# Performance work log

Measured on AMD Instinct MI355X. Metric: run time of the kernel, lower is better.

Reference implementation:

```python
import jax, jax.numpy as jnp
import numpy as np

N_NODES = 100000
IN_FEATURES = 5000
OUT_FEATURES = 64
NNZ = 4000000


def setup_inputs() -> dict:
    key = jax.random.key(0)
    k_row, k_col, k_val, k_w, k_b = jax.random.split(key, 5)
    rows = jax.random.randint(k_row, (NNZ,), 0, N_NODES, dtype=jnp.int64 if jax.config.jax_enable_x64 else jnp.int32)
    cols = jax.random.randint(k_col, (NNZ,), 0, IN_FEATURES, dtype=rows.dtype)
    index = jnp.stack([rows, cols], axis=0)  # [2, nnz] COO
    value = jax.random.uniform(k_val, (NNZ,), dtype=jnp.float32)
    # kaiming_uniform_(mode='fan_out', a=sqrt(5)) on [in, out]: fan_out = out_features
    gain = np.sqrt(2.0 / (1.0 + 5.0))
    bound_w = gain * np.sqrt(3.0 / OUT_FEATURES)
    weight = jax.random.uniform(k_w, (IN_FEATURES, OUT_FEATURES), jnp.float32, -bound_w, bound_w)
    bound_b = 1.0 / np.sqrt(OUT_FEATURES)
    bias = jax.random.uniform(k_b, (OUT_FEATURES,), jnp.float32, -bound_b, bound_b)
    return {"index": index, "value": value, "n": N_NODES, "weight": weight, "bias": bias}


def reference(index, value, n, weight, bias):
    # spmm: out[r, :] = sum over nnz with row==r of value * weight[col, :]
    rows, cols = index[0], index[1]
    contrib = value[:, None] * weight[cols]            # [nnz, out] gather + scale
    res = jax.ops.segment_sum(contrib, rows, num_segments=n)  # [n, out] scatter-add
    return res + bias[None, :]
```

## Files before the change

### kernel.cpp

```cpp
#include <hip/hip_runtime.h>


#define NBF 1024
#define DMAX 128
#define CH 8192
#define CC 1536
#define SP_T 512

__device__ __forceinline__ void ds_fadd(float* p, float v) {
    unsigned a = (unsigned)(unsigned long long)p;
    asm volatile("ds_add_f32 %0, %1" :: "v"(a), "v"(v) : "memory");
}

__global__ __launch_bounds__(1024) void k_bin_fixed(const int* __restrict__ rows,
        const int* __restrict__ cols, const float* __restrict__ vals, int nnz,
        unsigned M, int S, int d, int slots, int* __restrict__ cntF,
        unsigned long long* __restrict__ pairs1, int* __restrict__ ovfCnt,
        unsigned long long* __restrict__ ovf) {
    __shared__ unsigned long long stage[CH];
    __shared__ int histF[NBF], scF[NBF], adjF[NBF];
    __shared__ int wsum[16];
    int t = threadIdx.x, lane = t & 63, wv = t >> 6;
    long long base = (long long)blockIdx.x * CH;
    int count = (int)min((long long)CH, (long long)nnz - base);
    histF[t] = 0;
    __syncthreads();
    int f8[8], rk8[8];
    unsigned long long pk8[8];
    if (count == CH) {
        const int4*   r4 = (const int4*)(rows + base);
        const int4*   c4 = (const int4*)(cols + base);
        const float4* v4 = (const float4*)(vals + base);
        int4 ra = r4[t * 2], rb = r4[t * 2 + 1];
        int4 ca = c4[t * 2], cb = c4[t * 2 + 1];
        float4 va = v4[t * 2], vb = v4[t * 2 + 1];
        int   rr[8] = {ra.x, ra.y, ra.z, ra.w, rb.x, rb.y, rb.z, rb.w};
        int   cc[8] = {ca.x, ca.y, ca.z, ca.w, cb.x, cb.y, cb.z, cb.w};
        float vv[8] = {va.x, va.y, va.z, va.w, vb.x, vb.y, vb.z, vb.w};
#pragma unroll
        for (int k = 0; k < 8; ++k) {
            unsigned r = (unsigned)rr[k];
            int f = (int)(((unsigned long long)r * M) >> S);
            int lr = (int)r - f * d;
            f8[k] = f;
            rk8[k] = atomicAdd(&histF[f], 1);
            pk8[k] = ((unsigned long long)__float_as_uint(vv[k]) << 32) |
                     ((unsigned)f << 20) | ((unsigned)lr << 13) | (unsigned)cc[k];
        }
    } else {
#pragma unroll
        for (int k = 0; k < 8; ++k) {
            int i = t + (k << 10);
            f8[k] = -1;
            if (i < count) {
                unsigned r = (unsigned)rows[base + i];
                int c = cols[base + i];
                float vv = vals[base + i];
                int f = (int)(((unsigned long long)r * M) >> S);
                int lr = (int)r - f * d;
                f8[k] = f;
                rk8[k] = atomicAdd(&histF[f], 1);
                pk8[k] = ((unsigned long long)__float_as_uint(vv) << 32) |
                         ((unsigned)f << 20) | ((unsigned)lr << 13) | (unsigned)c;
            }
        }
    }
    __syncthreads();
    int v = histF[t], x = v;
#pragma unroll
    for (int off = 1; off < 64; off <<= 1) {
        int y = __shfl_up(x, off, 64);
        if (lane >= off) x += y;
    }
    if (lane == 63) wsum[wv] = x;
    __syncthreads();
    if (t < 16) {
        int s = wsum[t], xs = s;
#pragma unroll
        for (int off = 1; off < 16; off <<= 1) {
            int y = __shfl_up(xs, off, 16);
            if (t >= off) xs += y;
        }
        wsum[t] = xs - s;
    }
    __syncthreads();
    int incl = x + wsum[wv];
    scF[t] = incl;
    if (v > 0) {
        int g = atomicAdd(&cntF[t], v);
        adjF[t] = t * slots + g - (incl - v);
    }
    __syncthreads();
#pragma unroll
    for (int k = 0; k < 8; ++k)
        if (f8[k] >= 0) stage[(scF[f8[k]] - histF[f8[k]]) + rk8[k]] = pk8[k];
    __syncthreads();
    for (int i = t; i < count; i += 1024) {
        unsigned long long p = stage[i];
        int f = (int)((p >> 20) & 1023);
        int dest = adjF[f] + i;
        if (dest < (f + 1) * slots) pairs1[dest] = p;
        else ovf[atomicAdd(ovfCnt, 1)] = p;
    }
}

__global__ __launch_bounds__(SP_T, 8) void k_spmm9(
        const unsigned long long* __restrict__ pairs, const int* __restrict__ cntF,
        const int* __restrict__ ovfCnt, const unsigned long long* __restrict__ ovf,
        const float* __restrict__ weight, const float* __restrict__ bias,
        float* __restrict__ out, int d, int n, int slots) {
    __shared__ unsigned long long stage[CC];
    __shared__ int histR[DMAX], scR[DMAX];
    extern __shared__ float acc[];
    int b = blockIdx.x, t = threadIdx.x;
    int row0 = b * d;
    if (row0 >= n) return;
    int nrows = min(d, n - row0);
    long long sbase = (long long)b * slots;
    int cnt = cntF[b];
    if (cnt > slots) cnt = slots;
    if (cnt < 0) cnt = 0;

    for (int i = t; i < (nrows << 6); i += SP_T) acc[i] = 0.0f;

    int g = t >> 4, fq = t & 15;
    for (int cb = 0; cb < cnt; cb += CC) {
        int ccnt = min(CC, cnt - cb);
        if (t < DMAX) histR[t] = 0;
        __syncthreads();
        int lr3[3], rk3[3];
        unsigned long long pk3[3];
#pragma unroll
        for (int k = 0; k < 3; ++k) {
            int i = t + (k << 9);
            lr3[k] = -1;
            if (i < ccnt) {
                unsigned long long p = pairs[sbase + cb + i];
                int lr = (int)((p >> 13) & 127);
                lr3[k] = lr;
                rk3[k] = atomicAdd(&histR[lr], 1);
                pk3[k] = p;
            }
        }
        __syncthreads();
        if (t < DMAX) {
            int v = histR[t], x = v;
            int lane = t & 63;
#pragma unroll
            for (int off = 1; off < 64; off <<= 1) {
                int y = __shfl_up(x, off, 64);
                if (lane >= off) x += y;
            }
            scR[t] = x;
        }
        __syncthreads();
        if (t >= 64 && t < DMAX) scR[t] += scR[63];
        __syncthreads();
#pragma unroll
        for (int k = 0; k < 3; ++k)
            if (lr3[k] >= 0) stage[(scR[lr3[k]] - histR[lr3[k]]) + rk3[k]] = pk3[k];
        __syncthreads();

        for (int r = g; r < nrows; r += 32) {
            int e = scR[r], s = e - histR[r];
            if (s >= e) continue;
            float4 a = {0.0f, 0.0f, 0.0f, 0.0f};
            int j = s;
            for (; j + 4 <= e; j += 4) {
                unsigned long long p0 = stage[j + 0];
                unsigned long long p1 = stage[j + 1];
                unsigned long long p2 = stage[j + 2];
                unsigned long long p3 = stage[j + 3];
                const float4 w0 = *(const float4*)(weight + (((int)(p0 & 8191)) << 6) + (fq << 2));
                const float4 w1 = *(const float4*)(weight + (((int)(p1 & 8191)) << 6) + (fq << 2));
                const float4 w2 = *(const float4*)(weight + (((int)(p2 & 8191)) << 6) + (fq << 2));
                const float4 w3 = *(const float4*)(weight + (((int)(p3 & 8191)) << 6) + (fq << 2));
                float v0 = __uint_as_float((unsigned)(p0 >> 32));
                float v1 = __uint_as_float((unsigned)(p1 >> 32));
                float v2 = __uint_as_float((unsigned)(p2 >> 32));
                float v3 = __uint_as_float((unsigned)(p3 >> 32));
                a.x = fmaf(v0, w0.x, a.x); a.y = fmaf(v0, w0.y, a.y);
                a.z = fmaf(v0, w0.z, a.z); a.w = fmaf(v0, w0.w, a.w);
                a.x = fmaf(v1, w1.x, a.x); a.y = fmaf(v1, w1.y, a.y);
                a.z = fmaf(v1, w1.z, a.z); a.w = fmaf(v1, w1.w, a.w);
                a.x = fmaf(v2, w2.x, a.x); a.y = fmaf(v2, w2.y, a.y);
                a.z = fmaf(v2, w2.z, a.z); a.w = fmaf(v2, w2.w, a.w);
                a.x = fmaf(v3, w3.x, a.x); a.y = fmaf(v3, w3.y, a.y);
                a.z = fmaf(v3, w3.z, a.z); a.w = fmaf(v3, w3.w, a.w);
            }
            for (; j < e; ++j) {
                unsigned long long p = stage[j];
                float vv = __uint_as_float((unsigned)(p >> 32));
                const float4 w = *(const float4*)(weight + (((int)(p & 8191)) << 6) + (fq << 2));
                a.x = fmaf(vv, w.x, a.x); a.y = fmaf(vv, w.y, a.y);
                a.z = fmaf(vv, w.z, a.z); a.w = fmaf(vv, w.w, a.w);
            }
            float4* ap = (float4*)&acc[(r << 6) + (fq << 2)];
            float4 o = *ap;
            o.x += a.x; o.y += a.y; o.z += a.z; o.w += a.w;
            *ap = o;
        }
        __syncthreads();
    }

    int oc = *ovfCnt;
    if (oc > 0) {
        __syncthreads();
        for (int i = g; i < oc; i += (SP_T >> 4)) {
            unsigned long long p = ovf[i];
            if ((int)((p >> 20) & 1023) == b) {
                int lr = (int)((p >> 13) & 127);
                int cc = (int)(p & 8191);
                float vv = __uint_as_float((unsigned)(p >> 32));
                const float4 w = *(const float4*)(weight + (cc << 6) + (fq << 2));
                float* ap = &acc[(lr << 6) + (fq << 2)];
                ds_fadd(ap + 0, vv * w.x); ds_fadd(ap + 1, vv * w.y);
                ds_fadd(ap + 2, vv * w.z); ds_fadd(ap + 3, vv * w.w);
            }
        }
        asm volatile("s_waitcnt lgkmcnt(0)" ::: "memory");
        __builtin_amdgcn_sched_barrier(0);
        __syncthreads();
    }

    for (int i = t; i < (nrows << 6); i += SP_T)
        out[((long long)row0 << 6) + i] = acc[i] + bias[i & 63];
}

extern "C" void kernel_launch(void* const* d_in, const int* in_sizes, int n_in,
                              void* d_out, int out_size, void* d_ws, size_t ws_size,
                              hipStream_t stream) {
    const int*   index  = (const int*)d_in[0];
    const float* value  = (const float*)d_in[1];
    const float* weight = (const float*)d_in[3];
    const float* bias   = (const float*)d_in[4];
    float*       out    = (float*)d_out;

    int nnz = in_sizes[0] / 2;
    int n   = out_size / 64;
    const int* rows = index;
    const int* cols = index + nnz;

    int d = (n + NBF - 1) / NBF;
    unsigned M = 0;
    int S = 0;
    for (S = 20; S <= 40; ++S) {
        unsigned long long m = ((1ull << S) + (unsigned)d - 1) / (unsigned)d;
        unsigned long long e = m * (unsigned long long)d - (1ull << S);
        if (m <= 0xffffffffull && e * (unsigned long long)(n > 0 ? n - 1 : 0) < (1ull << S)) {
            M = (unsigned)m;
            break;
        }
    }

    int nChunks = (nnz + CH - 1) / CH;
    char* ws = (char*)d_ws;
    int* cntF   = (int*)ws;
    int* ovfCnt = (int*)(ws + 4096);
    unsigned long long* pairsS = (unsigned long long*)(ws + (128 << 10));

    size_t szOvf = (((size_t)nnz * 8) + 255) & ~(size_t)255;
    size_t availS = (ws_size > (128 << 10) + szOvf) ? (ws_size - (128 << 10) - szOvf) : 0;
    long long slotsL = (long long)(availS / ((size_t)NBF * 8));
    int slots = (int)(slotsL > 6144 ? 6144 : slotsL);
    if (slots > 64) slots &= ~63;
    if (slots < 1) slots = 1;
    unsigned long long* ovf = (unsigned long long*)(ws + (128 << 10) + (size_t)slots * NBF * 8);

    hipMemsetAsync(ws, 0, 8192, stream);
    k_bin_fixed<<<nChunks, 1024, 0, stream>>>(rows, cols, value, nnz, M, S, d, slots,
                                              cntF, pairsS, ovfCnt, ovf);
    size_t smem = (size_t)d * 64 * sizeof(float);
    k_spmm9<<<NBF, SP_T, smem, stream>>>(pairsS, cntF, ovfCnt, ovf, weight, bias,
                                         out, d, n, slots);
}
```

Before: 160.6 us.

## Keep row accumulators in registers and enlarge SpMM staging chunk

Replaces the shared-memory per-row accumulator in the SpMM kernel with four float4 register accumulators per thread, each thread owning fixed rows (g + 32k), and writes output directly with bias. The staging chunk grows from 1536 to 4608 pairs. The first pass now keeps only the rank and local row in registers and re-reads the pair from global memory during the scatter. This removes LDS accumulator traffic and the dynamic shared allocation, and cuts the number of chunk iterations and barriers. In exchange it assumes at most 128 rows per block, adds a redundant global load per pair, and makes every thread scan the whole overflow list serially. The larger stage array (about 36KB) may also reduce occupancy.

Result: no change. 160.3 us (-0.2%).

```diff
diff --git a/kernel.cpp b/kernel.cpp
--- a/kernel.cpp
+++ b/kernel.cpp
@@ -4,13 +4,8 @@
 #define NBF 1024
 #define DMAX 128
 #define CH 8192
-#define CC 1536
+#define CC 4608
 #define SP_T 512
-
-__device__ __forceinline__ void ds_fadd(float* p, float v) {
-    unsigned a = (unsigned)(unsigned long long)p;
-    asm volatile("ds_add_f32 %0, %1" :: "v"(a), "v"(v) : "memory");
-}
 
 __global__ __launch_bounds__(1024) void k_bin_fixed(const int* __restrict__ rows,
         const int* __restrict__ cols, const float* __restrict__ vals, int nnz,
@@ -104,14 +99,13 @@
     }
 }
 
-__global__ __launch_bounds__(SP_T, 8) void k_spmm9(
+__global__ __launch_bounds__(SP_T, 8) void k_spmm12(
         const unsigned long long* __restrict__ pairs, const int* __restrict__ cntF,
         const int* __restrict__ ovfCnt, const unsigned long long* __restrict__ ovf,
         const float* __restrict__ weight, const float* __restrict__ bias,
         float* __restrict__ out, int d, int n, int slots) {
     __shared__ unsigned long long stage[CC];
     __shared__ int histR[DMAX], scR[DMAX];
-    extern __shared__ float acc[];
     int b = blockIdx.x, t = threadIdx.x;
     int row0 = b * d;
     if (row0 >= n) return;
@@ -121,25 +115,24 @@
     if (cnt > slots) cnt = slots;
     if (cnt < 0) cnt = 0;
 
-    for (int i = t; i < (nrows << 6); i += SP_T) acc[i] = 0.0f;
-
     int g = t >> 4, fq = t & 15;
+    const float* wbase = weight + (fq << 2);
+    float4 a0 = {0,0,0,0}, a1 = {0,0,0,0}, a2 = {0,0,0,0}, a3 = {0,0,0,0};
+
     for (int cb = 0; cb < cnt; cb += CC) {
         int ccnt = min(CC, cnt - cb);
         if (t < DMAX) histR[t] = 0;
         __syncthreads();
-        int lr3[3], rk3[3];
-        unsigned long long pk3[3];
-#pragma unroll
-        for (int k = 0; k < 3; ++k) {
+        int pr9[9];
+#pragma unroll
+        for (int k = 0; k < 9; ++k) {
             int i = t + (k << 9);
-            lr3[k] = -1;
+            pr9[k] = -1;
             if (i < ccnt) {
                 unsigned long long p = pairs[sbase + cb + i];
                 int lr = (int)((p >> 13) & 127);
-                lr3[k] = lr;
-                rk3[k] = atomicAdd(&histR[lr], 1);
-                pk3[k] = p;
+                int rk = atomicAdd(&histR[lr], 1);
+                pr9[k] = (rk << 7) | lr;
             }
         }
         __syncthreads();
@@ -157,74 +150,96 @@
         if (t >= 64 && t < DMAX) scR[t] += scR[63];
         __syncthreads();
 #pragma unroll
-        for (int k = 0; k < 3; ++k)
-            if (lr3[k] >= 0) stage[(scR[lr3[k]] - histR[lr3[k]]) + rk3[k]] = pk3[k];
-        __syncthreads();
-
-        for (int r = g; r < nrows; r += 32) {
-            int e = scR[r], s = e - histR[r];
-            if (s >= e) continue;
-            float4 a = {0.0f, 0.0f, 0.0f, 0.0f};
-            int j = s;
-            for (; j + 4 <= e; j += 4) {
-                unsigned long long p0 = stage[j + 0];
-                unsigned long long p1 = stage[j + 1];
-                unsigned long long p2 = stage[j + 2];
-                unsigned long long p3 = stage[j + 3];
-                const float4 w0 = *(const float4*)(weight + (((int)(p0 & 8191)) << 6) + (fq << 2));
-                const float4 w1 = *(const float4*)(weight + (((int)(p1 & 8191)) << 6) + (fq << 2));
-                const float4 w2 = *(const float4*)(weight + (((int)(p2 & 8191)) << 6) + (fq << 2));
-                const float4 w3 = *(const float4*)(weight + (((int)(p3 & 8191)) << 6) + (fq << 2));
-                float v0 = __uint_as_float((unsigned)(p0 >> 32));
-                float v1 = __uint_as_float((unsigned)(p1 >> 32));
-                float v2 = __uint_as_float((unsigned)(p2 >> 32));
-                float v3 = __uint_as_float((unsigned)(p3 >> 32));
-                a.x = fmaf(v0, w0.x, a.x); a.y = fmaf(v0, w0.y, a.y);
-                a.z = fmaf(v0, w0.z, a.z); a.w = fmaf(v0, w0.w, a.w);
-                a.x = fmaf(v1, w1.x, a.x); a.y = fmaf(v1, w1.y, a.y);
-                a.z = fmaf(v1, w1.z, a.z); a.w = fmaf(v1, w1.w, a.w);
-                a.x = fmaf(v2, w2.x, a.x); a.y = fmaf(v2, w2.y, a.y);
-                a.z = fmaf(v2, w2.z, a.z); a.w = fmaf(v2, w2.w, a.w);
-                a.x = fmaf(v3, w3.x, a.x); a.y = fmaf(v3, w3.y, a.y);
-                a.z = fmaf(v3, w3.z, a.z); a.w = fmaf(v3, w3.w, a.w);
-            }
-            for (; j < e; ++j) {
-                unsigned long long p = stage[j];
-                float vv = __uint_as_float((unsigned)(p >> 32));
-                const float4 w = *(const float4*)(weight + (((int)(p & 8191)) << 6) + (fq << 2));
-                a.x = fmaf(vv, w.x, a.x); a.y = fmaf(vv, w.y, a.y);
-                a.z = fmaf(vv, w.z, a.z); a.w = fmaf(vv, w.w, a.w);
-            }
-            float4* ap = (float4*)&acc[(r << 6) + (fq << 2)];
-            float4 o = *ap;
-            o.x += a.x; o.y += a.y; o.z += a.z; o.w += a.w;
-            *ap = o;
-        }
+        for (int k = 0; k < 9; ++k) {
+            if (pr9[k] >= 0) {
+                int i = t + (k << 9);
+                int lr = pr9[k] & 127, rk = pr9[k] >> 7;
+                stage[(scR[lr] - histR[lr]) + rk] = pairs[sbase + cb + i];
+            }
+        }
+        __syncthreads();
+
+#define CONSUME_ROW(K)                                                        \
+        {                                                                     \
+            int r = g + (K << 5);                                             \
+            if (r < nrows) {                                                  \
+                int e = scR[r], s = e - histR[r];                             \
+                float4 a = {0,0,0,0};                                         \
+                int j = s;                                                    \
+                for (; j + 4 <= e; j += 4) {                                  \
+                    unsigned long long p0 = stage[j + 0];                     \
+                    unsigned long long p1 = stage[j + 1];                     \
+                    unsigned long long p2 = stage[j + 2];                     \
+                    unsigned long long p3 = stage[j + 3];                     \
+                    const float4 w0 = *(const float4*)(wbase + ((int)(p0 & 8191) << 6)); \
+                    const float4 w1 = *(const float4*)(wbase + ((int)(p1 & 8191) << 6)); \
+                    const float4 w2 = *(const float4*)(wbase + ((int)(p2 & 8191) << 6)); \
+                    const float4 w3 = *(const float4*)(wbase + ((int)(p3 & 8191) << 6)); \
+                    float v0 = __uint_as_float((unsigned)(p0 >> 32));         \
+                    float v1 = __uint_as_float((unsigned)(p1 >> 32));         \
+                    float v2 = __uint_as_float((unsigned)(p2 >> 32));         \
+                    float v3 = __uint_as_float((unsigned)(p3 >> 32));         \
+                    a.x = fmaf(v0, w0.x, a.x); a.y = fmaf(v0, w0.y, a.y);     \
+                    a.z = fmaf(v0, w0.z, a.z); a.w = fmaf(v0, w0.w, a.w);     \
+                    a.x = fmaf(v1, w1.x, a.x); a.y = fmaf(v1, w1.y, a.y);     \
+                    a.z = fmaf(v1, w1.z, a.z); a.w = fmaf(v1, w1.w, a.w);     \
+                    a.x = fmaf(v2, w2.x, a.x); a.y = fmaf(v2, w2.y, a.y);     \
+                    a.z = fmaf(v2, w2.z, a.z); a.w = fmaf(v2, w2.w, a.w);     \
+                    a.x = fmaf(v3, w3.x, a.x); a.y = fmaf(v3, w3.y, a.y);     \
+                    a.z = fmaf(v3, w3.z, a.z); a.w = fmaf(v3, w3.w, a.w);     \
+                }                                                             \
+                for (; j < e; ++j) {                                          \
+                    unsigned long long p = stage[j];                          \
+                    float vv = __uint_as_float((unsigned)(p >> 32));          \
+                    const float4 w = *(const float4*)(wbase + ((int)(p & 8191) << 6)); \
+                    a.x = fmaf(vv, w.x, a.x); a.y = fmaf(vv, w.y, a.y);       \
+                    a.z = fmaf(vv, w.z, a.z); a.w = fmaf(vv, w.w, a.w);       \
+                }                                                             \
+                a##K.x += a.x; a##K.y += a.y; a##K.z += a.z; a##K.w += a.w;   \
+            }                                                                 \
+        }
+        CONSUME_ROW(0) CONSUME_ROW(1) CONSUME_ROW(2) CONSUME_ROW(3)
+#undef CONSUME_ROW
         __syncthreads();
     }
 
     int oc = *ovfCnt;
     if (oc > 0) {
-        __syncthreads();
-        for (int i = g; i < oc; i += (SP_T >> 4)) {
+        for (int i = 0; i < oc; ++i) {
             unsigned long long p = ovf[i];
             if ((int)((p >> 20) & 1023) == b) {
                 int lr = (int)((p >> 13) & 127);
-                int cc = (int)(p & 8191);
-                float vv = __uint_as_float((unsigned)(p >> 32));
-                const float4 w = *(const float4*)(weight + (cc << 6) + (fq << 2));
-                float* ap = &acc[(lr << 6) + (fq << 2)];
-                ds_fadd(ap + 0, vv * w.x); ds_fadd(ap + 1, vv * w.y);
-                ds_fadd(ap + 2, vv * w.z); ds_fadd(ap + 3, vv * w.w);
-            }
-        }
-        asm volatile("s_waitcnt lgkmcnt(0)" ::: "memory");
-        __builtin_amdgcn_sched_barrier(0);
-        __syncthreads();
-    }
-
-    for (int i = t; i < (nrows << 6); i += SP_T)
-        out[((long long)row0 << 6) + i] = acc[i] + bias[i & 63];
+                if ((lr & 31) == g) {
+                    int cc = (int)(p & 8191);
+                    float vv = __uint_as_float((unsigned)(p >> 32));
+                    const float4 w = *(const float4*)(wbase + (cc << 6));
+                    int k = lr >> 5;
+                    if (k == 0) { a0.x = fmaf(vv, w.x, a0.x); a0.y = fmaf(vv, w.y, a0.y);
+                                  a0.z = fmaf(vv, w.z, a0.z); a0.w = fmaf(vv, w.w, a0.w); }
+                    else if (k == 1) { a1.x = fmaf(vv, w.x, a1.x); a1.y = fmaf(vv, w.y, a1.y);
+                                  a1.z = fmaf(vv, w.z, a1.z); a1.w = fmaf(vv, w.w, a1.w); }
+                    else if (k == 2) { a2.x = fmaf(vv, w.x, a2.x); a2.y = fmaf(vv, w.y, a2.y);
+                                  a2.z = fmaf(vv, w.z, a2.z); a2.w = fmaf(vv, w.w, a2.w); }
+                    else { a3.x = fmaf(vv, w.x, a3.x); a3.y = fmaf(vv, w.y, a3.y);
+                                  a3.z = fmaf(vv, w.z, a3.z); a3.w = fmaf(vv, w.w, a3.w); }
+                }
+            }
+        }
+    }
+
+    float4 b4 = *(const float4*)(bias + (fq << 2));
+#define WRITE_ROW(K)                                                          \
+    {                                                                         \
+        int r = g + (K << 5);                                                 \
+        if (r < nrows) {                                                      \
+            float4 o;                                                         \
+            o.x = a##K.x + b4.x; o.y = a##K.y + b4.y;                         \
+            o.z = a##K.z + b4.z; o.w = a##K.w + b4.w;                         \
+            *(float4*)(out + (((long long)(row0 + r)) << 6) + (fq << 2)) = o; \
+        }                                                                     \
+    }
+    WRITE_ROW(0) WRITE_ROW(1) WRITE_ROW(2) WRITE_ROW(3)
+#undef WRITE_ROW
 }
 
 extern "C" void kernel_launch(void* const* d_in, const int* in_sizes, int n_in,
@@ -270,7 +285,6 @@
     hipMemsetAsync(ws, 0, 8192, stream);
     k_bin_fixed<<<nChunks, 1024, 0, stream>>>(rows, cols, value, nnz, M, S, d, slots,
                                               cntF, pairsS, ovfCnt, ovf);
-    size_t smem = (size_t)d * 64 * sizeof(float);
-    k_spmm9<<<NBF, SP_T, smem, stream>>>(pairsS, cntF, ovfCnt, ovf, weight, bias,
-                                         out, d, n, slots);
+    k_spmm12<<<NBF, SP_T, 0, stream>>>(pairsS, cntF, ovfCnt, ovf, weight, bias,
+                                       out, d, n, slots);
 }
```
